# Kernel optimization log

Measured on AMD Instinct MI355X. Metric: run time of the kernel, lower is better.

Reference implementation:

```python
import jax, jax.numpy as jnp
import numpy as np

Q = 2.0
TEMPERATURE = 1.0
EXP = 1.0 / (Q - 1.0)  # exponent 1/(q-1); q=2 -> sparsemax-style projection
N_BISECT_ITERS = 50    # enough for xtol ~ 1e-6 over an interval of width ~ (u_max - u_min + 10)


def setup_inputs() -> dict:
    key = jax.random.key(0)
    k_x, k_w1, k_w2 = jax.random.split(key, 3)
    B, D, H, E = 8192, 4096, 256, 64
    x = jax.random.normal(k_x, (B, D), dtype=jnp.float32)
    w1 = jax.random.normal(k_w1, (D, H), dtype=jnp.float32) * 0.02
    b1 = jnp.zeros((H,), dtype=jnp.float32)
    w2 = jax.random.normal(k_w2, (H, E), dtype=jnp.float32) * 0.05
    b2 = jnp.zeros((E,), dtype=jnp.float32)
    return {"x": x, "w1": w1, "b1": b1, "w2": w2, "b2": b2}


def _bisect_tau(us):
    # us: [B, E] = utilities / temperature. Find per-row tau with sum(relu(us - tau)**EXP) = 1.
    lo = jnp.min(us, axis=-1) - 10.0   # constraint(lo) > 0
    hi = jnp.max(us, axis=-1)          # constraint(hi) = -1 < 0

    def body(i, carry):
        lo, hi = carry
        mid = 0.5 * (lo + hi)
        f = jnp.sum(jnp.maximum(us - mid[..., None], 0.0) ** EXP, axis=-1) - 1.0
        pos = f > 0.0  # constraint is decreasing in tau: root is above mid
        return (jnp.where(pos, mid, lo), jnp.where(pos, hi, mid))

    lo, hi = jax.lax.fori_loop(0, N_BISECT_ITERS, body, (lo, hi))
    return 0.5 * (lo + hi)  # [B]


def reference(x, w1, b1, w2, b2):
    # utility_net (Dropout is identity in eval mode)
    h = jax.nn.relu(x @ w1 + b1)            # [B, 256]
    utilities = h @ w2 + b2                  # [B, E]
    us = utilities / TEMPERATURE
    # tau is found by root-finding on detached values in the original (.item()),
    # so it is a constant w.r.t. differentiation.
    tau = jax.lax.stop_gradient(_bisect_tau(jax.lax.stop_gradient(us)))
    p = jnp.maximum(us - tau[..., None], 0.0) ** EXP   # [B, E]
    p = p / (jnp.sum(p, axis=-1, keepdims=True) + 1e-8)
    return p
```

## Files before the change

### kernel.cpp

```cpp
#include <hip/hip_runtime.h>
#include <stdint.h>

typedef _Float16 f16;
typedef _Float16 f16x8 __attribute__((ext_vector_type(8)));
typedef _Float16 f16x4 __attribute__((ext_vector_type(4)));
typedef float f32x4 __attribute__((ext_vector_type(4)));

#define D_DIM 4096
#define H_DIM 256
#define E_DIM 64
#define BM 32
#define BK 64
#define KSPLIT 4
#define NKT2 16

__global__ void pack_kernel(const float* __restrict__ w1, f16* __restrict__ w1s,
                            const float* __restrict__ w2, f16* __restrict__ w2s) {
  const int b = blockIdx.x;
  const int t = threadIdx.x;
  if (b < 512) {
    const int u = b * 256 + t;
    const int lane = u & 63;
    const int kk = (u >> 6) & 1;
    const int c16 = (u >> 7) & 15;
    const int kt = u >> 11;
    const int g = lane >> 4, r = lane & 15;
    const int k0 = kt * 64 + kk * 32 + g * 8;
    const int col = c16 * 16 + r;
    f16x8 o;
#pragma unroll
    for (int j = 0; j < 8; ++j) o[j] = (f16)w1[(size_t)(k0 + j) * H_DIM + col];
    *(f16x8*)(w1s + (size_t)u * 8) = o;
  } else {
    const int u = (b - 512) * 256 + t;
    const int lane = u & 63;
    const int ks = (u >> 6) & 7;
    const int cg = u >> 9;
    const int g = lane >> 4, r = lane & 15;
    const int k0 = ks * 32 + g * 8;
    const int col = cg * 16 + r;
    f16x8 o;
#pragma unroll
    for (int j = 0; j < 8; ++j) o[j] = (f16)w2[(size_t)(k0 + j) * E_DIM + col];
    *(f16x8*)(w2s + (size_t)u * 8) = o;
  }
}

__launch_bounds__(512)
__global__ void gemm1_splitk_kernel(const float* __restrict__ x,
                                    const f16* __restrict__ w1s,
                                    float* __restrict__ hpart) {
  __shared__ __align__(16) f16 As0[BM * BK];
  __shared__ __align__(16) f16 As1[BM * BK];

  const int t = threadIdx.x;
  const int lane = t & 63;
  const int wn = t >> 6;
  const int g = lane >> 4, r = lane & 15;
  const int bid = blockIdx.x;
  const int ks = bid & 3;
  const int rb = bid >> 2;
  const int brow = rb * BM;

  const int a_row = t >> 4;
  const int a_col = (t & 15) << 2;
  const int a_sw = a_col ^ ((a_row & 7) << 3);
  const float* xrow = x + (size_t)(brow + a_row) * D_DIM + ks * 1024 + a_col;
  const f16* bptr = w1s + (size_t)ks * 16 * 16384 + (size_t)(wn * 2) * 1024 + lane * 8;

  f32x4 acc[2][2] = {{{0.f,0.f,0.f,0.f},{0.f,0.f,0.f,0.f}},
                     {{0.f,0.f,0.f,0.f},{0.f,0.f,0.f,0.f}}};
  f16x8 B0[4], B1[4];
  float4 xE, xO;

#define LDX(kt) (*(const float4*)(xrow + (kt) * 64))
#define LDB(kt, B)                                                  \
  {                                                                 \
    const f16* p_ = bptr + (size_t)(kt) * 16384;                    \
    (B)[0] = *(const f16x8*)(p_);                                   \
    (B)[1] = *(const f16x8*)(p_ + 512);                             \
    (B)[2] = *(const f16x8*)(p_ + 1024);                            \
    (B)[3] = *(const f16x8*)(p_ + 1536);                            \
  }
#define STW(As, v)                                                  \
  {                                                                 \
    f16x4 hv_;                                                      \
    hv_[0] = (f16)(v).x; hv_[1] = (f16)(v).y;                       \
    hv_[2] = (f16)(v).z; hv_[3] = (f16)(v).w;                       \
    *(f16x4*)((As) + a_row * 64 + a_sw) = hv_;                      \
  }
#define COMP(As, B)                                                            \
  {                                                                            \
    _Pragma("unroll") for (int kk = 0; kk < 2; ++kk) {                         \
      const int kb_ = kk * 32 + g * 8;                                         \
      _Pragma("unroll") for (int rh = 0; rh < 2; ++rh) {                       \
        const int arow_ = rh * 16 + r;                                         \
        const f16x8 af_ =                                                      \
            *(const f16x8*)((As) + arow_ * 64 + (kb_ ^ ((arow_ & 7) << 3)));   \
        _Pragma("unroll") for (int ch = 0; ch < 2; ++ch) {                     \
          acc[rh][ch] = __builtin_amdgcn_mfma_f32_16x16x32_f16(                \
              af_, (B)[kk + ch * 2], acc[rh][ch], 0, 0, 0);                    \
        }                                                                      \
      }                                                                        \
    }                                                                          \
  }
#define BAR()                                          \
  asm volatile("s_waitcnt lgkmcnt(0)" ::: "memory");   \
  __builtin_amdgcn_s_barrier();

  {
    float4 t0 = LDX(0);
    LDB(0, B0);
    LDB(1, B1);
    xE = LDX(1);
    xO = LDX(2);
    STW(As0, t0);
    BAR();
  }

#pragma unroll 1
  for (int s = 0; s < NKT2; s += 2) {
    STW(As1, xE);
    xE = LDX(s + 3 < NKT2 ? s + 3 : NKT2 - 1);
    COMP(As0, B0);
    LDB(s + 2 < NKT2 ? s + 2 : NKT2 - 1, B0);
    BAR();
    STW(As0, xO);
    xO = LDX(s + 4 < NKT2 ? s + 4 : NKT2 - 1);
    COMP(As1, B1);
    LDB(s + 3 < NKT2 ? s + 3 : NKT2 - 1, B1);
    BAR();
  }

  float* hp = hpart + (size_t)bid * (BM * H_DIM);
#pragma unroll
  for (int rh = 0; rh < 2; ++rh)
#pragma unroll
    for (int ch = 0; ch < 2; ++ch) {
      const int col = wn * 32 + ch * 16 + r;
#pragma unroll
      for (int j = 0; j < 4; ++j) {
        const int row = rh * 16 + g * 4 + j;
        hp[row * H_DIM + col] = acc[rh][ch][j];
      }
    }
}

__launch_bounds__(512)
__global__ void reduce_fused_kernel(const float* __restrict__ hpart,
                                    const float* __restrict__ b1,
                                    const f16* __restrict__ w2s,
                                    const float* __restrict__ b2,
                                    float* __restrict__ out) {
  __shared__ __align__(16) char smem[24576];
  f16* h_lds = (f16*)smem;
  float* u_lds = (float*)(smem + 16384);

  const int t = threadIdx.x;
  const int lane = t & 63;
  const int wn = t >> 6;
  const int g = lane >> 4, r = lane & 15;
  const int brow = blockIdx.x * BM;

  const float* base = hpart + (size_t)blockIdx.x * (KSPLIT * BM * H_DIM);
  float4 s[4];
#pragma unroll
  for (int i = 0; i < 4; ++i)
    s[i] = *(const float4*)(base + (size_t)(i * 512 + t) * 4);
#pragma unroll
  for (int c = 1; c < KSPLIT; ++c) {
    const float* cb = base + (size_t)c * (BM * H_DIM);
#pragma unroll
    for (int i = 0; i < 4; ++i) {
      const float4 v = *(const float4*)(cb + (size_t)(i * 512 + t) * 4);
      s[i].x += v.x; s[i].y += v.y; s[i].z += v.z; s[i].w += v.w;
    }
  }
#pragma unroll
  for (int i = 0; i < 4; ++i) {
    const int f = i * 512 + t;
    const int row = f >> 6;
    const int col = (f & 63) << 2;
    const float4 bv = *(const float4*)(b1 + col);
    f16x4 hv;
    hv[0] = (f16)fmaxf(s[i].x + bv.x, 0.f);
    hv[1] = (f16)fmaxf(s[i].y + bv.y, 0.f);
    hv[2] = (f16)fmaxf(s[i].z + bv.z, 0.f);
    hv[3] = (f16)fmaxf(s[i].w + bv.w, 0.f);
    *(f16x4*)(h_lds + row * 256 + (col ^ ((row & 7) << 3))) = hv;
  }
  __syncthreads();

  const int rh2 = wn & 1;
  const int cg = wn >> 1;
  f32x4 acc2 = {0.f, 0.f, 0.f, 0.f};
  const f16* w2p = w2s + (size_t)(cg * 8) * 512 + lane * 8;
#pragma unroll
  for (int ksi = 0; ksi < 8; ++ksi) {
    const int arow = rh2 * 16 + r;
    const int kb = ksi * 32 + g * 8;
    const f16x8 af = *(const f16x8*)(h_lds + arow * 256 + (kb ^ ((arow & 7) << 3)));
    const f16x8 bf = *(const f16x8*)(w2p + ksi * 512);
    acc2 = __builtin_amdgcn_mfma_f32_16x16x32_f16(af, bf, acc2, 0, 0, 0);
  }
  {
    const int col = cg * 16 + r;
    const float bias = b2[col];
#pragma unroll
    for (int j = 0; j < 4; ++j) {
      const int row = rh2 * 16 + g * 4 + j;
      u_lds[row * 64 + col] = acc2[j] + bias;
    }
  }
  __syncthreads();

  const int srow = wn * 4 + (lane >> 4);
  const int scol = (lane & 15) << 2;
  const float4 uv = *(const float4*)(u_lds + srow * 64 + scol);
  float u0 = uv.x, u1 = uv.y, u2 = uv.z, u3 = uv.w;

  float mx = fmaxf(fmaxf(u0, u1), fmaxf(u2, u3));
  float mn = fminf(fminf(u0, u1), fminf(u2, u3));
#pragma unroll
  for (int m = 1; m < 16; m <<= 1) {
    mx = fmaxf(mx, __shfl_xor(mx, m));
    mn = fminf(mn, __shfl_xor(mn, m));
  }
  float lo = mn - 10.0f, hi = mx;
#pragma unroll 1
  for (int it = 0; it < 32; ++it) {
    const float mid = 0.5f * (lo + hi);
    float sm = fmaxf(u0 - mid, 0.f) + fmaxf(u1 - mid, 0.f) +
               fmaxf(u2 - mid, 0.f) + fmaxf(u3 - mid, 0.f);
#pragma unroll
    for (int m = 1; m < 16; m <<= 1) sm += __shfl_xor(sm, m);
    const bool pos = (sm - 1.0f) > 0.0f;
    lo = pos ? mid : lo;
    hi = pos ? hi : mid;
  }
  const float tau = 0.5f * (lo + hi);
  const float p0 = fmaxf(u0 - tau, 0.f);
  const float p1 = fmaxf(u1 - tau, 0.f);
  const float p2 = fmaxf(u2 - tau, 0.f);
  const float p3 = fmaxf(u3 - tau, 0.f);
  float sum = p0 + p1 + p2 + p3;
#pragma unroll
  for (int m = 1; m < 16; m <<= 1) sum += __shfl_xor(sum, m);
  const float inv = 1.0f / (sum + 1e-8f);
  float4 pv;
  pv.x = p0 * inv; pv.y = p1 * inv; pv.z = p2 * inv; pv.w = p3 * inv;
  *(float4*)(out + (size_t)(brow + srow) * E_DIM + scol) = pv;
}

extern "C" void kernel_launch(void* const* d_in, const int* in_sizes, int n_in,
                              void* d_out, int out_size, void* d_ws, size_t ws_size,
                              hipStream_t stream) {
  const float* x  = (const float*)d_in[0];
  const float* w1 = (const float*)d_in[1];
  const float* b1 = (const float*)d_in[2];
  const float* w2 = (const float*)d_in[3];
  const float* b2 = (const float*)d_in[4];
  float* out = (float*)d_out;

  char* wsb = (char*)d_ws;
  f16* w1s = (f16*)wsb;
  f16* w2s = (f16*)(wsb + (2u << 20));
  float* hpart = (float*)(wsb + (4u << 20));

  pack_kernel<<<520, 256, 0, stream>>>(w1, w1s, w2, w2s);
  gemm1_splitk_kernel<<<1024, 512, 0, stream>>>(x, w1s, hpart);
  reduce_fused_kernel<<<256, 512, 0, stream>>>(hpart, b1, w2s, b2, out);
}
```

Measured before the change: 60.25 us.

## Enlarge GEMM1 row tile to 128 with 2x4 warp grid and 4x4 MFMA fragments

Raises the GEMM1 block tile from 32 to 128 rows. The eight waves form a 2x4 grid, and each wave computes a 64x64 sub-tile with 16 accumulators, so every loaded B fragment is reused across four row fragments. The aim is to cut redundant global reads of the packed W1 by four and improve MFMA density. In exchange there are only 256 blocks for 256 CUs split four ways along K, and much higher register pressure. The partial-sum layout is changed to per-K-split slices, and the reduce kernel is adapted to match.

```diff
diff --git a/kernel.cpp b/kernel.cpp
--- a/kernel.cpp
+++ b/kernel.cpp
@@ -9,10 +9,11 @@
 #define D_DIM 4096
 #define H_DIM 256
 #define E_DIM 64
-#define BM 32
+#define BM 128
 #define BK 64
 #define KSPLIT 4
 #define NKT2 16
+#define HP_SLICE (8192 * 256)
 
 __global__ void pack_kernel(const float* __restrict__ w1, f16* __restrict__ w1s,
                             const float* __restrict__ w2, f16* __restrict__ w2s) {
@@ -46,60 +47,68 @@
   }
 }
 
-__launch_bounds__(512)
+__launch_bounds__(512, 2)
 __global__ void gemm1_splitk_kernel(const float* __restrict__ x,
                                     const f16* __restrict__ w1s,
                                     float* __restrict__ hpart) {
-  __shared__ __align__(16) f16 As0[BM * BK];
-  __shared__ __align__(16) f16 As1[BM * BK];
+  __shared__ __align__(16) f16 buf0[BM * BK];
+  __shared__ __align__(16) f16 buf1[BM * BK];
 
   const int t = threadIdx.x;
   const int lane = t & 63;
   const int wn = t >> 6;
+  const int wm = wn >> 2;
+  const int wc = wn & 3;
   const int g = lane >> 4, r = lane & 15;
   const int bid = blockIdx.x;
   const int ks = bid & 3;
-  const int rb = bid >> 2;
-  const int brow = rb * BM;
-
-  const int a_row = t >> 4;
-  const int a_col = (t & 15) << 2;
-  const int a_sw = a_col ^ ((a_row & 7) << 3);
-  const float* xrow = x + (size_t)(brow + a_row) * D_DIM + ks * 1024 + a_col;
-  const f16* bptr = w1s + (size_t)ks * 16 * 16384 + (size_t)(wn * 2) * 1024 + lane * 8;
-
-  f32x4 acc[2][2] = {{{0.f,0.f,0.f,0.f},{0.f,0.f,0.f,0.f}},
-                     {{0.f,0.f,0.f,0.f},{0.f,0.f,0.f,0.f}}};
-  f16x8 B0[4], B1[4];
-  float4 xE, xO;
-
-#define LDX(kt) (*(const float4*)(xrow + (kt) * 64))
-#define LDB(kt, B)                                                  \
-  {                                                                 \
-    const f16* p_ = bptr + (size_t)(kt) * 16384;                    \
-    (B)[0] = *(const f16x8*)(p_);                                   \
-    (B)[1] = *(const f16x8*)(p_ + 512);                             \
-    (B)[2] = *(const f16x8*)(p_ + 1024);                            \
-    (B)[3] = *(const f16x8*)(p_ + 1536);                            \
-  }
-#define STW(As, v)                                                  \
-  {                                                                 \
-    f16x4 hv_;                                                      \
-    hv_[0] = (f16)(v).x; hv_[1] = (f16)(v).y;                       \
-    hv_[2] = (f16)(v).z; hv_[3] = (f16)(v).w;                       \
-    *(f16x4*)((As) + a_row * 64 + a_sw) = hv_;                      \
-  }
-#define COMP(As, B)                                                            \
+  const int brow = (bid >> 2) * BM;
+
+  const float* xb = x + (size_t)(brow + (t >> 4)) * D_DIM + ks * 1024 + ((t & 15) << 2);
+  const int stw_swz = (((t & 15) << 2) ^ (((t >> 4) & 7) << 3));
+  const int stw_row0 = (t >> 4);
+
+  const f16* bptr = w1s + (size_t)ks * (16 * 16384) + (size_t)(wc * 8) * 512 + lane * 8;
+
+  f32x4 acc[4][4];
+#pragma unroll
+  for (int mf = 0; mf < 4; ++mf)
+#pragma unroll
+    for (int nf = 0; nf < 4; ++nf) acc[mf][nf] = (f32x4){0.f, 0.f, 0.f, 0.f};
+
+  f16x8 BE[8], BO[8];
+  float4 xA[4], xB[4], xP[4];
+
+#define LDX(kt, xr)                                                     \
+  {                                                                     \
+    _Pragma("unroll") for (int i = 0; i < 4; ++i)                       \
+      (xr)[i] = *(const float4*)(xb + (size_t)i * (32 * D_DIM) + (kt) * 64); \
+  }
+#define LDB(kt, B)                                                      \
+  {                                                                     \
+    const f16* p_ = bptr + (size_t)(kt) * 16384;                        \
+    _Pragma("unroll") for (int q = 0; q < 8; ++q)                       \
+      (B)[q] = *(const f16x8*)(p_ + q * 512);                           \
+  }
+#define STW(dst, xr)                                                    \
+  {                                                                     \
+    _Pragma("unroll") for (int i = 0; i < 4; ++i) {                     \
+      f16x4 hv_;                                                        \
+      hv_[0] = (f16)(xr)[i].x; hv_[1] = (f16)(xr)[i].y;                 \
+      hv_[2] = (f16)(xr)[i].z; hv_[3] = (f16)(xr)[i].w;                 \
+      *(f16x4*)((dst) + (i * 32 + stw_row0) * 64 + stw_swz) = hv_;      \
+    }                                                                   \
+  }
+#define COMP(buf, B)                                                           \
   {                                                                            \
     _Pragma("unroll") for (int kk = 0; kk < 2; ++kk) {                         \
-      const int kb_ = kk * 32 + g * 8;                                         \
-      _Pragma("unroll") for (int rh = 0; rh < 2; ++rh) {                       \
-        const int arow_ = rh * 16 + r;                                         \
-        const f16x8 af_ =                                                      \
-            *(const f16x8*)((As) + arow_ * 64 + (kb_ ^ ((arow_ & 7) << 3)));   \
-        _Pragma("unroll") for (int ch = 0; ch < 2; ++ch) {                     \
-          acc[rh][ch] = __builtin_amdgcn_mfma_f32_16x16x32_f16(                \
-              af_, (B)[kk + ch * 2], acc[rh][ch], 0, 0, 0);                    \
+      const int kb_ = (kk * 32 + g * 8) ^ ((r & 7) << 3);                      \
+      _Pragma("unroll") for (int mf = 0; mf < 4; ++mf) {                       \
+        const int row_ = wm * 64 + mf * 16 + r;                                \
+        const f16x8 af_ = *(const f16x8*)((buf) + row_ * 64 + kb_);            \
+        _Pragma("unroll") for (int nf = 0; nf < 4; ++nf) {                     \
+          acc[mf][nf] = __builtin_amdgcn_mfma_f32_16x16x32_f16(                \
+              af_, (B)[nf * 2 + kk], acc[mf][nf], 0, 0, 0);                    \
         }                                                                      \
       }                                                                        \
     }                                                                          \
@@ -109,39 +118,52 @@
   __builtin_amdgcn_s_barrier();
 
   {
-    float4 t0 = LDX(0);
-    LDB(0, B0);
-    LDB(1, B1);
-    xE = LDX(1);
-    xO = LDX(2);
-    STW(As0, t0);
+    LDX(0, xP);
+    LDB(0, BE);
+    LDB(1, BO);
+    LDX(1, xA);
+    LDX(2, xB);
+    STW(buf0, xP);
     BAR();
   }
 
 #pragma unroll 1
-  for (int s = 0; s < NKT2; s += 2) {
-    STW(As1, xE);
-    xE = LDX(s + 3 < NKT2 ? s + 3 : NKT2 - 1);
-    COMP(As0, B0);
-    LDB(s + 2 < NKT2 ? s + 2 : NKT2 - 1, B0);
+  for (int it = 0; it < NKT2 / 2; ++it) {
+    const int kt = it * 2;
+    STW(buf1, xA);
+    {
+      int sx = kt + 3; if (sx > NKT2 - 1) sx = NKT2 - 1;
+      LDX(sx, xA);
+    }
+    COMP(buf0, BE);
+    {
+      int sb = kt + 2; if (sb > NKT2 - 1) sb = NKT2 - 1;
+      LDB(sb, BE);
+    }
     BAR();
-    STW(As0, xO);
-    xO = LDX(s + 4 < NKT2 ? s + 4 : NKT2 - 1);
-    COMP(As1, B1);
-    LDB(s + 3 < NKT2 ? s + 3 : NKT2 - 1, B1);
+    STW(buf0, xB);
+    {
+      int sx = kt + 4; if (sx > NKT2 - 1) sx = NKT2 - 1;
+      LDX(sx, xB);
+    }
+    COMP(buf1, BO);
+    {
+      int sb = kt + 3; if (sb > NKT2 - 1) sb = NKT2 - 1;
+      LDB(sb, BO);
+    }
     BAR();
   }
 
-  float* hp = hpart + (size_t)bid * (BM * H_DIM);
-#pragma unroll
-  for (int rh = 0; rh < 2; ++rh)
-#pragma unroll
-    for (int ch = 0; ch < 2; ++ch) {
-      const int col = wn * 32 + ch * 16 + r;
+  float* hp = hpart + (size_t)ks * HP_SLICE + (size_t)brow * H_DIM;
+#pragma unroll
+  for (int mf = 0; mf < 4; ++mf)
+#pragma unroll
+    for (int nf = 0; nf < 4; ++nf) {
+      const int col = wc * 64 + nf * 16 + r;
 #pragma unroll
       for (int j = 0; j < 4; ++j) {
-        const int row = rh * 16 + g * 4 + j;
-        hp[row * H_DIM + col] = acc[rh][ch][j];
+        const int row = wm * 64 + mf * 16 + g * 4 + j;
+        hp[(size_t)row * H_DIM + col] = acc[mf][nf][j];
       }
     }
 }
@@ -160,16 +182,16 @@
   const int lane = t & 63;
   const int wn = t >> 6;
   const int g = lane >> 4, r = lane & 15;
-  const int brow = blockIdx.x * BM;
-
-  const float* base = hpart + (size_t)blockIdx.x * (KSPLIT * BM * H_DIM);
+  const int brow = blockIdx.x * 32;
+
+  const float* base = hpart + (size_t)brow * H_DIM;
   float4 s[4];
 #pragma unroll
   for (int i = 0; i < 4; ++i)
     s[i] = *(const float4*)(base + (size_t)(i * 512 + t) * 4);
 #pragma unroll
   for (int c = 1; c < KSPLIT; ++c) {
-    const float* cb = base + (size_t)c * (BM * H_DIM);
+    const float* cb = base + (size_t)c * HP_SLICE;
 #pragma unroll
     for (int i = 0; i < 4; ++i) {
       const float4 v = *(const float4*)(cb + (size_t)(i * 512 + t) * 4);
@@ -268,6 +290,6 @@
   float* hpart = (float*)(wsb + (4u << 20));
 
   pack_kernel<<<520, 256, 0, stream>>>(w1, w1s, w2, w2s);
-  gemm1_splitk_kernel<<<1024, 512, 0, stream>>>(x, w1s, hpart);
+  gemm1_splitk_kernel<<<256, 512, 0, stream>>>(x, w1s, hpart);
   reduce_fused_kernel<<<256, 512, 0, stream>>>(hpart, b1, w2s, b2, out);
 }
```

Result: faster. 57.86 us (-4.0%).
